# Optimization experiments

Measured on AMD Instinct MI355X. Metric: run time of the kernel, lower is better.

Reference implementation:

```python
import jax, jax.numpy as jnp
import numpy as np

N, P, T, D = 25000, 100000, 4, 128
DIN = 4 * D + 4  # 516
LEAKY = 0.001


def setup_inputs() -> dict:
    key = jax.random.key(0)
    ks = jax.random.split(key, 12)
    inp = {
        "coords": jax.random.normal(ks[0], (N, T, 3), jnp.float32),
        "propers": jax.random.randint(ks[1], (P, 4), 0, N, jnp.int64),
        "encoded": jax.random.normal(ks[2], (N, D), jnp.float32),
        "t": jax.random.uniform(ks[3], (T,), jnp.float32),
        "answer": jax.random.normal(ks[4], (N, T, 3), jnp.float32),
        # AggregateMLP(516 -> 128 -> 128 -> 128 -> 2), LeakyReLU(0.001) between
        "W0": jax.random.normal(ks[5], (DIN, D), jnp.float32) / np.sqrt(DIN),
        "b0": jnp.zeros((D,), jnp.float32),
        "W1": jax.random.normal(ks[6], (D, D), jnp.float32) / np.sqrt(D),
        "b1": jnp.zeros((D,), jnp.float32),
        "W2": jax.random.normal(ks[7], (D, D), jnp.float32) / np.sqrt(D),
        "b2": jnp.zeros((D,), jnp.float32),
        "W3": jax.random.normal(ks[8], (D, 2), jnp.float32) / np.sqrt(D),
        "b3": jnp.zeros((2,), jnp.float32),
    }
    return inp


def _forward(coords, propers, encoded, t, answer, W0, b0, W1, b1, W2, b2, W3, b3):
    p0, p1, p2, p3 = propers[:, 0], propers[:, 1], propers[:, 2], propers[:, 3]
    c0, c1, c2, c3 = coords[p0], coords[p1], coords[p2], coords[p3]  # [P,T,3]
    u1 = c1 - c0
    u2 = c2 - c1
    u3 = c3 - c2
    u1xu2 = jnp.cross(u1, u2, axis=-1)
    u2xu3 = jnp.cross(u2, u3, axis=-1)
    u2_norm = jnp.linalg.norm(u2, axis=-1, keepdims=True)
    u1yu2 = u1 * u2_norm
    theta = jnp.arctan2((u1yu2 * u2xu3).sum(-1), (u1xu2 * u2xu3).sum(-1))  # [P,T]
    dr = c0 - c3  # [P,T,3]
    dl = jnp.sqrt(jnp.clip(jnp.square(dr).sum(-1), 1e-12))  # [P,T]
    dh = dr / dl[..., None]

    Pn, Tn = propers.shape[0], t.shape[0]
    bcast = lambda e: jnp.broadcast_to(e[:, None, :], (Pn, Tn, e.shape[-1]))
    feats = jnp.concatenate(
        [
            bcast(encoded[p0]),
            bcast(encoded[p1]),
            bcast(encoded[p2]),
            bcast(encoded[p3]),
            jnp.broadcast_to(t.reshape(1, Tn, 1), (Pn, Tn, 1)),
            jnp.sin(theta)[..., None],
            jnp.cos(theta)[..., None],
            dl[..., None],
        ],
        axis=2,
    )  # [P,T,516]

    h = jax.nn.leaky_relu(feats @ W0 + b0, LEAKY)
    h = jax.nn.leaky_relu(h @ W1 + b1, LEAKY)
    h = jax.nn.leaky_relu(h @ W2 + b2, LEAKY)
    delta = h @ W3 + b3  # [P,T,2]

    out = answer.at[p0].add(-0.5 * delta[:, :, 0:1] * dh)
    out = out.at[p3].add(0.5 * delta[:, :, 1:2] * dh)
    return out


def reference(coords, propers, encoded, t, answer, W0, b0, W1, b1, W2, b2, W3, b3):
    return _forward(coords, propers, encoded, t, answer, W0, b0, W1, b1, W2, b2, W3, b3)
```

## Files before the change

kernel.cpp:

```cpp
#include <hip/hip_runtime.h>
#include <hip/hip_bf16.h>

#define NN 25000
#define PP 100000
#define TT 4
#define DD 128
#define LEAKY 0.001f

#define PB 32
#define ROWS 128

typedef __bf16 bf16;
typedef __bf16 bf16x8 __attribute__((ext_vector_type(8)));
typedef float  f32x4  __attribute__((ext_vector_type(4)));

#define OFF_W0SW  0u
#define OFF_W1SW  131072u
#define OFF_W2SW  163840u
#define OFF_W3SW  196608u
#define OFF_WTB   200704u
#define OFF_W5B   201728u
#define OFF_E     202496u
#define WS_END    25802496u

#define PR_W0SW  65536
#define PR_W1SW  16384
#define PR_W2SW  16384
#define PR_W3SW  2048
#define PR_WTB   512
#define PR_W5B   384
#define PR_COPY4 75000
#define PR_TOTAL (PR_W0SW + PR_W1SW + PR_W2SW + PR_W3SW + PR_WTB + PR_W5B + PR_COPY4)

__global__ __launch_bounds__(256) void prep_kernel(
    const float* __restrict__ W0, const float* __restrict__ W1,
    const float* __restrict__ W2, const float* __restrict__ W3,
    const float* __restrict__ answer, const float* __restrict__ tvec,
    const float* __restrict__ b0,
    bf16* __restrict__ W0sw, bf16* __restrict__ W1sw, bf16* __restrict__ W2sw,
    bf16* __restrict__ W3sw, bf16* __restrict__ WtB, bf16* __restrict__ W5B,
    float* __restrict__ out)
{
    int idx = blockIdx.x * 256 + threadIdx.x;
    if (idx < PR_W0SW) {
        int j = idx & 7, lane = (idx >> 3) & 63, c = idx >> 9;
        int fr = lane & 15, quad = lane >> 4;
        int kc = c & 15, iwv = c >> 4;
        int k = kc * 32 + quad * 8 + j;
        W0sw[idx] = (bf16)W0[k * 128 + iwv * 16 + fr];
        return;
    }
    idx -= PR_W0SW;
    if (idx < PR_W1SW) {
        int j = idx & 7, lane = (idx >> 3) & 63, c = idx >> 9;
        int fr = lane & 15, quad = lane >> 4;
        int kc = c & 3, nt = c >> 2;
        int k = kc * 32 + quad * 8 + j;
        W1sw[idx] = (bf16)W1[k * 128 + nt * 16 + fr];
        return;
    }
    idx -= PR_W1SW;
    if (idx < PR_W2SW) {
        int j = idx & 7, lane = (idx >> 3) & 63, c = idx >> 9;
        int fr = lane & 15, quad = lane >> 4;
        int kc = c & 3, nt = c >> 2;
        int k = kc * 32 + quad * 8 + j;
        W2sw[idx] = (bf16)W2[k * 128 + nt * 16 + fr];
        return;
    }
    idx -= PR_W2SW;
    if (idx < PR_W3SW) {
        int j = idx & 7, lane = (idx >> 3) & 63, kc = idx >> 9;
        int fr = lane & 15, quad = lane >> 4;
        int k = kc * 32 + quad * 8 + j;
        W3sw[idx] = (fr < 2) ? (bf16)W3[k * 2 + fr] : (bf16)0.0f;
        return;
    }
    idx -= PR_W3SW;
    if (idx < PR_WTB) {
        int t = idx >> 7, j = idx & 127;
        WtB[idx] = (bf16)(tvec[t] * W0[512 * 128 + j] + b0[j]);
        return;
    }
    idx -= PR_WTB;
    if (idx < PR_W5B) {
        W5B[idx] = (bf16)W0[(513 + (idx >> 7)) * 128 + (idx & 127)];
        return;
    }
    idx -= PR_W5B;
    if (idx < PR_COPY4) { ((float4*)out)[idx] = ((const float4*)answer)[idx]; }
}

__global__ __launch_bounds__(512) void prep_e_kernel(
    const float* __restrict__ encoded, const bf16* __restrict__ W0sw,
    bf16* __restrict__ E)
{
    __shared__ bf16 sA[128][136];
    __shared__ bf16 sT[128][40];
    const int tid = threadIdx.x;
    const int row0 = (blockIdx.x >> 2) * 128;
    const int ntb  = blockIdx.x & 3;
    for (int c = tid; c < 4096; c += 512) {
        int row = c >> 5, seg = c & 31;
        int rr = row0 + row; if (rr >= NN) rr = NN - 1;
        float4 v = *(const float4*)(encoded + (size_t)rr * 128 + seg * 4);
        bf16 pk[4] = {(bf16)v.x, (bf16)v.y, (bf16)v.z, (bf16)v.w};
        *(uint2*)(&sA[row][seg * 4]) = *(const uint2*)pk;
    }
    __syncthreads();
    const int wv = tid >> 6, lane = tid & 63;
    const int fr = lane & 15, quad = lane >> 4;
    const bf16* aBase = &sA[wv * 16 + fr][quad * 8];
    bf16x8 aFv[4];
    #pragma unroll
    for (int kcc = 0; kcc < 4; ++kcc) aFv[kcc] = *(const bf16x8*)(aBase + kcc * 32);
    const int orow = tid >> 2, oseg = tid & 3;
    #pragma unroll
    for (int i = 0; i < 4; ++i) {
        #pragma unroll
        for (int ntl = 0; ntl < 2; ++ntl) {
            int nt = ntb * 2 + ntl;
            f32x4 acc = {0.f, 0.f, 0.f, 0.f};
            #pragma unroll
            for (int kcc = 0; kcc < 4; ++kcc) {
                bf16x8 bF = *(const bf16x8*)(W0sw + ((size_t)nt * 16 + i * 4 + kcc) * 512 + lane * 8);
                acc = __builtin_amdgcn_mfma_f32_16x16x32_bf16(aFv[kcc], bF, acc, 0, 0, 0);
            }
            #pragma unroll
            for (int reg = 0; reg < 4; ++reg)
                sT[wv * 16 + quad * 4 + reg][ntl * 16 + fr] = (bf16)acc[reg];
        }
        __syncthreads();
        if (row0 + orow < NN)
            *(bf16x8*)(E + ((size_t)i * NN + row0 + orow) * 128 + ntb * 32 + oseg * 8) =
                *(const bf16x8*)(&sT[orow][oseg * 8]);
        __syncthreads();
    }
}

__global__ __launch_bounds__(512, 6) void main_kernel(
    const float* __restrict__ coords, const int* __restrict__ propers,
    const float* __restrict__ b1, const float* __restrict__ b2,
    const float* __restrict__ b3,
    const bf16* __restrict__ E, const bf16* __restrict__ W1sw,
    const bf16* __restrict__ W2sw, const bf16* __restrict__ W3sw,
    const bf16* __restrict__ WtB, const bf16* __restrict__ W5B,
    float* __restrict__ out)
{
    __shared__ __align__(16) bf16 sH[8][16][136];
    __shared__ float sScr[8][16][6];
    __shared__ int   sNd[8][8];

    const int tid  = threadIdx.x;
    const int wv   = tid >> 6, lane = tid & 63;
    const int fr   = lane & 15, quad = lane >> 4;
    const int pw   = blockIdx.x * PB + wv * 4;

#define LGKM0() asm volatile("s_waitcnt lgkmcnt(0)" ::: "memory")

    int4 pv = *(const int4*)(propers + (size_t)(pw + quad) * 4);
    bf16x8 e0 = *(const bf16x8*)(E + ((size_t)0 * NN + pv.x) * 128 + fr * 8);
    bf16x8 e1 = *(const bf16x8*)(E + ((size_t)1 * NN + pv.y) * 128 + fr * 8);
    bf16x8 e2 = *(const bf16x8*)(E + ((size_t)2 * NN + pv.z) * 128 + fr * 8);
    bf16x8 e3 = *(const bf16x8*)(E + ((size_t)3 * NN + pv.w) * 128 + fr * 8);
    if (fr == 0) { sNd[wv][quad * 2] = pv.x; sNd[wv][quad * 2 + 1] = pv.w; }
    bf16x8 w3v = *(const bf16x8*)(W5B + 0 * 128 + fr * 8);
    bf16x8 w4v = *(const bf16x8*)(W5B + 1 * 128 + fr * 8);
    bf16x8 w5v = *(const bf16x8*)(W5B + 2 * 128 + fr * 8);

    float snl = 0.f, csl = 1.f, dll = 0.f;
    if (lane < 16) {
        int pp_ = lane >> 2, t = lane & 3;
        int4 pg = *(const int4*)(propers + (size_t)(pw + pp_) * 4);
        const float* c0 = coords + (size_t)pg.x * 12 + t * 3;
        const float* c1 = coords + (size_t)pg.y * 12 + t * 3;
        const float* c2 = coords + (size_t)pg.z * 12 + t * 3;
        const float* c3 = coords + (size_t)pg.w * 12 + t * 3;
        float u1x = c1[0]-c0[0], u1y = c1[1]-c0[1], u1z = c1[2]-c0[2];
        float u2x = c2[0]-c1[0], u2y = c2[1]-c1[1], u2z = c2[2]-c1[2];
        float u3x = c3[0]-c2[0], u3y = c3[1]-c2[1], u3z = c3[2]-c2[2];
        float ax = u1y*u2z - u1z*u2y, ay = u1z*u2x - u1x*u2z, az = u1x*u2y - u1y*u2x;
        float bx = u2y*u3z - u2z*u3y, by = u2z*u3x - u2x*u3z, bz = u2x*u3y - u2y*u3x;
        float u2n = sqrtf(u2x*u2x + u2y*u2y + u2z*u2z);
        float num = u2n * (u1x*bx + u1y*by + u1z*bz);
        float den = ax*bx + ay*by + az*bz;
        float hyp = sqrtf(num*num + den*den);
        if (hyp > 1e-30f) { float ih = 1.0f / hyp; snl = num * ih; csl = den * ih; }
        else { snl = 0.0f; csl = 1.0f; }
        float drx = c0[0]-c3[0], dry = c0[1]-c3[1], drz = c0[2]-c3[2];
        dll = sqrtf(fmaxf(drx*drx + dry*dry + drz*drz, 1e-12f));
        float il = 1.0f / dll;
        sScr[wv][lane][0] = drx * il;
        sScr[wv][lane][1] = dry * il;
        sScr[wv][lane][2] = drz * il;
    }

    {
        float g[8], w3f[8], w4f[8], w5f[8];
        #pragma unroll
        for (int j = 0; j < 8; ++j) {
            g[j]   = (float)e0[j] + (float)e1[j] + (float)e2[j] + (float)e3[j];
            w3f[j] = (float)w3v[j]; w4f[j] = (float)w4v[j]; w5f[j] = (float)w5v[j];
        }
        #pragma unroll
        for (int t = 0; t < 4; ++t) {
            int r = quad * 4 + t;
            bf16x8 wtv = *(const bf16x8*)(WtB + t * 128 + fr * 8);
            float sn = __shfl(snl, r), cs = __shfl(csl, r), dl = __shfl(dll, r);
            bf16 hv[8];
            #pragma unroll
            for (int j = 0; j < 8; ++j) {
                float v = g[j] + (float)wtv[j] + sn * w3f[j] + cs * w4f[j] + dl * w5f[j];
                v = fmaxf(v, LEAKY * v);
                hv[j] = (bf16)v;
            }
            *(bf16x8*)(&sH[wv][r][fr * 8]) = *(const bf16x8*)hv;
        }
    }

#define DENSE_LAYER(Wsw, bvec)                                                  \
    {                                                                           \
        LGKM0();        \
        bf16x8 aF[4];                                                           \
        const bf16* aRow = &sH[wv][fr][quad * 8];                               \
        _Pragma("unroll")                                                       \
        for (int kc = 0; kc < 4; ++kc)                                          \
            aF[kc] = *(const bf16x8*)(aRow + kc * 32);                          \
        LGKM0();      \
        _Pragma("unroll")                                                       \
        for (int hh = 0; hh < 2; ++hh) {                                        \
            f32x4 acc[4];                                                       \
            _Pragma("unroll")                                                   \
            for (int nt = 0; nt < 4; ++nt) acc[nt] = (f32x4){0.f,0.f,0.f,0.f};  \
            _Pragma("unroll")                                                   \
            for (int kc = 0; kc < 4; ++kc) {                                    \
                _Pragma("unroll")                                               \
                for (int nt = 0; nt < 4; ++nt) {                                \
                    bf16x8 bF = *(const bf16x8*)(Wsw +                          \
                        ((size_t)((hh * 4 + nt) * 4 + kc)) * 512 + lane * 8);   \
                    acc[nt] = __builtin_amdgcn_mfma_f32_16x16x32_bf16(          \
                        aF[kc], bF, acc[nt], 0, 0, 0);                          \
                }                                                               \
            }                                                                   \
            _Pragma("unroll")                                                   \
            for (int nt = 0; nt < 4; ++nt) {                                    \
                int j = (hh * 4 + nt) * 16 + fr;                                \
                float bb = bvec[j];                                             \
                _Pragma("unroll")                                               \
                for (int reg = 0; reg < 4; ++reg) {                             \
                    float v = acc[nt][reg] + bb;                                \
                    v = fmaxf(v, LEAKY * v);                                    \
                    sH[wv][quad * 4 + reg][j] = (bf16)v;                        \
                }                                                               \
            }                                                                   \
        }                                                                       \
    }

    DENSE_LAYER(W1sw, b1)
    DENSE_LAYER(W2sw, b2)

    {
        LGKM0();
        bf16x8 aF[4];
        const bf16* aRow = &sH[wv][fr][quad * 8];
        #pragma unroll
        for (int kc = 0; kc < 4; ++kc)
            aF[kc] = *(const bf16x8*)(aRow + kc * 32);
        f32x4 dacc = {0.f, 0.f, 0.f, 0.f};
        #pragma unroll
        for (int kc = 0; kc < 4; ++kc) {
            bf16x8 bF = *(const bf16x8*)(W3sw + (size_t)kc * 512 + lane * 8);
            dacc = __builtin_amdgcn_mfma_f32_16x16x32_bf16(aF[kc], bF, dacc, 0, 0, 0);
        }
        if (fr < 2) {
            float bb = b3[fr];
            #pragma unroll
            for (int reg = 0; reg < 4; ++reg)
                sScr[wv][quad * 4 + reg][3 + fr] = dacc[reg] + bb;
        }
    }

    LGKM0();
    for (int idx = lane; idx < 96; idx += 64) {
        int r = idx / 6, c = idx - (idx / 6) * 6;
        int side = c / 3, ax = c - side * 3;
        int node = sNd[wv][(r >> 2) * 2 + side];
        float dval = (side ? 0.5f : -0.5f) * sScr[wv][r][3 + side];
        atomicAdd(out + (size_t)node * 12 + (r & 3) * 3 + ax, dval * sScr[wv][r][ax]);
    }
#undef DENSE_LAYER
#undef LGKM0
}

extern "C" void kernel_launch(void* const* d_in, const int* in_sizes, int n_in,
                              void* d_out, int out_size, void* d_ws, size_t ws_size,
                              hipStream_t stream) {
    const float* coords  = (const float*)d_in[0];
    const int*   propers = (const int*)d_in[1];
    const float* encoded = (const float*)d_in[2];
    const float* tvec    = (const float*)d_in[3];
    const float* answer  = (const float*)d_in[4];
    const float* W0 = (const float*)d_in[5];
    const float* b0 = (const float*)d_in[6];
    const float* W1 = (const float*)d_in[7];
    const float* b1 = (const float*)d_in[8];
    const float* W2 = (const float*)d_in[9];
    const float* b2 = (const float*)d_in[10];
    const float* W3 = (const float*)d_in[11];
    const float* b3 = (const float*)d_in[12];
    float* out = (float*)d_out;
    char* ws = (char*)d_ws;
    bf16* W0sw = (bf16*)(ws + OFF_W0SW);
    bf16* W1sw = (bf16*)(ws + OFF_W1SW);
    bf16* W2sw = (bf16*)(ws + OFF_W2SW);
    bf16* W3sw = (bf16*)(ws + OFF_W3SW);
    bf16* WtB  = (bf16*)(ws + OFF_WTB);
    bf16* W5B  = (bf16*)(ws + OFF_W5B);
    bf16* E    = (bf16*)(ws + OFF_E);

    int prep_blocks = (PR_TOTAL + 255) / 256;
    prep_kernel<<<prep_blocks, 256, 0, stream>>>(W0, W1, W2, W3, answer, tvec, b0,
                                                 W0sw, W1sw, W2sw, W3sw, WtB, W5B, out);
    prep_e_kernel<<<196 * 4, 512, 0, stream>>>(encoded, W0sw, E);
    main_kernel<<<PP / PB, 512, 0, stream>>>(coords, propers, b1, b2, b3,
                                             E, W1sw, W2sw, W3sw, WtB, W5B, out);
}
```

Baseline: 202.6 us.

## Stage MLP weights in LDS via global_load_lds and preload biases

The main kernel now copies W1 and W3 into a shared LDS buffer with direct global-to-LDS loads at kernel start. After layer 1 it reloads the same buffer with W2, separated by block barriers, so MFMA B-operands are read from LDS instead of global memory by every wave. Biases are preloaded into registers, and launch bounds drop from 6 to 4. The prep kernel's block barriers are replaced with wave-local LDS waits, since each wave reads only the rows it wrote. The roughly 36 KB of extra LDS per block and the new barriers may cut occupancy and serialize the W2 reload.

```diff
diff --git a/kernel.cpp b/kernel.cpp
--- a/kernel.cpp
+++ b/kernel.cpp
@@ -31,6 +31,14 @@
 #define PR_W5B   384
 #define PR_COPY4 75000
 #define PR_TOTAL (PR_W0SW + PR_W1SW + PR_W2SW + PR_W3SW + PR_WTB + PR_W5B + PR_COPY4)
+
+#define LGKM0() asm volatile("s_waitcnt lgkmcnt(0)" ::: "memory")
+
+__device__ __forceinline__ void gload_lds16(const void* g, void* l) {
+    __builtin_amdgcn_global_load_lds(
+        (const __attribute__((address_space(1))) void*)g,
+        (__attribute__((address_space(3))) void*)l, 16, 0, 0);
+}
 
 __global__ __launch_bounds__(256) void prep_kernel(
     const float* __restrict__ W0, const float* __restrict__ W1,
@@ -130,15 +138,15 @@
             for (int reg = 0; reg < 4; ++reg)
                 sT[wv * 16 + quad * 4 + reg][ntl * 16 + fr] = (bf16)acc[reg];
         }
-        __syncthreads();
+        LGKM0();
+        bf16x8 ev = *(const bf16x8*)(&sT[orow][oseg * 8]);
+        LGKM0();
         if (row0 + orow < NN)
-            *(bf16x8*)(E + ((size_t)i * NN + row0 + orow) * 128 + ntb * 32 + oseg * 8) =
-                *(const bf16x8*)(&sT[orow][oseg * 8]);
-        __syncthreads();
-    }
-}
-
-__global__ __launch_bounds__(512, 6) void main_kernel(
+            *(bf16x8*)(E + ((size_t)i * NN + row0 + orow) * 128 + ntb * 32 + oseg * 8) = ev;
+    }
+}
+
+__global__ __launch_bounds__(512, 4) void main_kernel(
     const float* __restrict__ coords, const int* __restrict__ propers,
     const float* __restrict__ b1, const float* __restrict__ b2,
     const float* __restrict__ b3,
@@ -148,6 +156,7 @@
     float* __restrict__ out)
 {
     __shared__ __align__(16) bf16 sH[8][16][136];
+    __shared__ __align__(16) bf16 sW[18432];
     __shared__ float sScr[8][16][6];
     __shared__ int   sNd[8][8];
 
@@ -156,7 +165,17 @@
     const int fr   = lane & 15, quad = lane >> 4;
     const int pw   = blockIdx.x * PB + wv * 4;
 
-#define LGKM0() asm volatile("s_waitcnt lgkmcnt(0)" ::: "memory")
+    {
+        const char* g1 = (const char*)W1sw;
+        char* l = (char*)&sW[0];
+        #pragma unroll
+        for (int r2 = 0; r2 < 4; ++r2)
+            gload_lds16(g1 + r2 * 8192 + wv * 1024 + lane * 16,
+                        l + r2 * 8192 + wv * 1024);
+        if (wv < 4)
+            gload_lds16((const char*)W3sw + wv * 1024 + lane * 16,
+                        l + 32768 + wv * 1024);
+    }
 
     int4 pv = *(const int4*)(propers + (size_t)(pw + quad) * 4);
     bf16x8 e0 = *(const bf16x8*)(E + ((size_t)0 * NN + pv.x) * 128 + fr * 8);
@@ -167,6 +186,14 @@
     bf16x8 w3v = *(const bf16x8*)(W5B + 0 * 128 + fr * 8);
     bf16x8 w4v = *(const bf16x8*)(W5B + 1 * 128 + fr * 8);
     bf16x8 w5v = *(const bf16x8*)(W5B + 2 * 128 + fr * 8);
+
+    float b1r[8], b2r[8];
+    #pragma unroll
+    for (int i = 0; i < 8; ++i) {
+        b1r[i] = b1[i * 16 + fr];
+        b2r[i] = b2[i * 16 + fr];
+    }
+    float b3r = (fr < 2) ? b3[fr] : 0.0f;
 
     float snl = 0.f, csl = 1.f, dll = 0.f;
     if (lane < 16) {
@@ -217,10 +244,11 @@
             *(bf16x8*)(&sH[wv][r][fr * 8]) = *(const bf16x8*)hv;
         }
     }
-
-#define DENSE_LAYER(Wsw, bvec)                                                  \
+    __syncthreads();
+
+#define DENSE_LAYER(BR)                                                         \
     {                                                                           \
-        LGKM0();        \
+        LGKM0();            \
         bf16x8 aF[4];                                                           \
         const bf16* aRow = &sH[wv][fr][quad * 8];                               \
         _Pragma("unroll")                                                       \
@@ -236,8 +264,8 @@
             for (int kc = 0; kc < 4; ++kc) {                                    \
                 _Pragma("unroll")                                               \
                 for (int nt = 0; nt < 4; ++nt) {                                \
-                    bf16x8 bF = *(const bf16x8*)(Wsw +                          \
-                        ((size_t)((hh * 4 + nt) * 4 + kc)) * 512 + lane * 8);   \
+                    bf16x8 bF = *(const bf16x8*)(sW +                           \
+                        ((hh * 4 + nt) * 4 + kc) * 512 + lane * 8);             \
                     acc[nt] = __builtin_amdgcn_mfma_f32_16x16x32_bf16(          \
                         aF[kc], bF, acc[nt], 0, 0, 0);                          \
                 }                                                               \
@@ -245,7 +273,7 @@
             _Pragma("unroll")                                                   \
             for (int nt = 0; nt < 4; ++nt) {                                    \
                 int j = (hh * 4 + nt) * 16 + fr;                                \
-                float bb = bvec[j];                                             \
+                float bb = BR[hh * 4 + nt];                                     \
                 _Pragma("unroll")                                               \
                 for (int reg = 0; reg < 4; ++reg) {                             \
                     float v = acc[nt][reg] + bb;                                \
@@ -256,8 +284,18 @@
         }                                                                       \
     }
 
-    DENSE_LAYER(W1sw, b1)
-    DENSE_LAYER(W2sw, b2)
+    DENSE_LAYER(b1r)
+    __syncthreads();
+    {
+        const char* g2 = (const char*)W2sw;
+        char* l = (char*)&sW[0];
+        #pragma unroll
+        for (int r2 = 0; r2 < 4; ++r2)
+            gload_lds16(g2 + r2 * 8192 + wv * 1024 + lane * 16,
+                        l + r2 * 8192 + wv * 1024);
+    }
+    __syncthreads();
+    DENSE_LAYER(b2r)
 
     {
         LGKM0();
@@ -269,14 +307,13 @@
         f32x4 dacc = {0.f, 0.f, 0.f, 0.f};
         #pragma unroll
         for (int kc = 0; kc < 4; ++kc) {
-            bf16x8 bF = *(const bf16x8*)(W3sw + (size_t)kc * 512 + lane * 8);
+            bf16x8 bF = *(const bf16x8*)(sW + 16384 + kc * 512 + lane * 8);
             dacc = __builtin_amdgcn_mfma_f32_16x16x32_bf16(aF[kc], bF, dacc, 0, 0, 0);
         }
         if (fr < 2) {
-            float bb = b3[fr];
             #pragma unroll
             for (int reg = 0; reg < 4; ++reg)
-                sScr[wv][quad * 4 + reg][3 + fr] = dacc[reg] + bb;
+                sScr[wv][quad * 4 + reg][3 + fr] = dacc[reg] + b3r;
         }
     }
 
@@ -289,7 +326,6 @@
         atomicAdd(out + (size_t)node * 12 + (r & 3) * 3 + ax, dval * sScr[wv][r][ax]);
     }
 #undef DENSE_LAYER
-#undef LGKM0
 }
 
 extern "C" void kernel_launch(void* const* d_in, const int* in_sizes, int n_in,
```

Measured after the change: 169.7 us. 16.2% less time.
